# Optimization experiments

Hardware: AMD Instinct MI355X
Metric: run time of the kernel (lower is better)

## Reference

```python
import jax, jax.numpy as jnp
import numpy as np

SEQ = 8192
IN_DIM = 1024
HIDDEN_DIM = 2048
N_EXPERTS = 8
TOPK = 2


def setup_inputs() -> dict:
    key = jax.random.key(0)
    ks = jax.random.split(key, 6)
    scale = 0.02
    inp = jax.random.normal(ks[0], (SEQ, IN_DIM), jnp.float32)
    weights = jax.random.uniform(ks[1], (SEQ, TOPK), jnp.float32)
    selections = jax.random.randint(ks[2], (SEQ, TOPK), 0, N_EXPERTS, jnp.int32)
    up_proj = jax.random.normal(ks[3], (HIDDEN_DIM * N_EXPERTS, IN_DIM), jnp.float32) * scale
    gate_proj = jax.random.normal(ks[4], (HIDDEN_DIM * N_EXPERTS, IN_DIM), jnp.float32) * scale
    down_proj = jax.random.normal(ks[5], (HIDDEN_DIM * N_EXPERTS, IN_DIM), jnp.float32) * scale
    return {"inp": inp, "weights": weights, "up_proj": up_proj,
            "gate_proj": gate_proj, "down_proj": down_proj, "selections": selections}


def reference(inp, weights, up_proj, gate_proj, down_proj, selections):
    seq, in_dim = inp.shape
    topk = selections.shape[-1]
    # dispatch: replicate each token topk times -> (seq*topk, in_dim)
    x = jnp.broadcast_to(inp[:, None, :], (seq, topk, in_dim)).reshape(-1, in_dim)
    e_ids = selections.reshape(-1)  # (seq*topk,) expert id per dispatched token
    W_up = up_proj.reshape(N_EXPERTS, HIDDEN_DIM, in_dim)
    W_gate = gate_proj.reshape(N_EXPERTS, HIDDEN_DIM, in_dim)
    W_down = down_proj.reshape(N_EXPERTS, HIDDEN_DIM, in_dim)
    out = jnp.zeros_like(x)
    # grouped (block-sparse) GEMM: loop over the small fixed expert set,
    # masking tokens not routed to this expert (gelu(0)*0 = 0, so math matches).
    for e in range(N_EXPERTS):
        mask = (e_ids == e)[:, None]
        xe = jnp.where(mask, x, 0.0)
        h = xe @ W_up[e].T        # (seq*topk, hidden)
        g = xe @ W_gate[e].T      # (seq*topk, hidden)
        out = out + jnp.where(mask, (jax.nn.gelu(g) * h) @ W_down[e], 0.0)
    # combine: weighted sum over topk expert outputs per token
    return (out.reshape(seq, topk, in_dim) * weights[:, :, None]).sum(axis=1)
```

## Files before the change

kernel.cpp:

```cpp
#include <hip/hip_runtime.h>


#define SEQ 8192
#define IN_DIM 1024
#define HID 2048
#define NEXP 8
#define TOPK 2
#define NSLOT (SEQ * TOPK)

#define BM 128
#define BK 64
#define BM1 256
#define MAX_T1 72

typedef unsigned short ushort_t;
typedef __bf16 bf16x8 __attribute__((ext_vector_type(8)));
typedef float f32x4 __attribute__((ext_vector_type(4)));

__device__ __forceinline__ ushort_t f2bf(float f) {
    union { float f; unsigned u; } v;
    v.f = f;
    unsigned r = v.u + 0x7FFFu + ((v.u >> 16) & 1u);
    return (ushort_t)(r >> 16);
}

__device__ __forceinline__ float gelu_tanh(float x) {
    float u = 0.7978845608028654f * x * (1.0f + 0.044715f * x * x);
    return x / (1.0f + __expf(-2.0f * u));
}

__device__ __forceinline__ void async16(const void* g, void* l) {
    __builtin_amdgcn_global_load_lds(
        (const __attribute__((address_space(1))) unsigned int*)g,
        (__attribute__((address_space(3))) unsigned int*)l, 16, 0, 0);
}

__global__ void cast_bf16_kernel(const float* __restrict__ in,
                                 ushort_t* __restrict__ out, int n) {
    int i = (blockIdx.x * blockDim.x + threadIdx.x) * 4;
    if (i >= n) return;
    float4 v = *(const float4*)(in + i);
    union { ushort_t u[4]; uint2 v; } o;
    o.u[0] = f2bf(v.x); o.u[1] = f2bf(v.y);
    o.u[2] = f2bf(v.z); o.u[3] = f2bf(v.w);
    *(uint2*)(out + i) = o.v;
}

__global__ void transpose_cast_kernel(const float* __restrict__ in,
                                      ushort_t* __restrict__ out) {
    __shared__ float tile[32][33];
    int e = blockIdx.z;
    int d0 = blockIdx.x * 32, h0 = blockIdx.y * 32;
    int tx = threadIdx.x & 31, ty = threadIdx.x >> 5;
    const float* src = in + (size_t)e * HID * IN_DIM;
    for (int j = 0; j < 32; j += 8)
        tile[ty + j][tx] = src[(size_t)(h0 + ty + j) * IN_DIM + d0 + tx];
    __syncthreads();
    ushort_t* dst = out + (size_t)e * IN_DIM * HID;
    for (int j = 0; j < 32; j += 8)
        dst[(size_t)(d0 + ty + j) * HID + h0 + tx] = f2bf(tile[tx][ty + j]);
}

__global__ void route_kernel(const int* __restrict__ sel,
                             const float* __restrict__ wts,
                             int* __restrict__ meta,
                             int* __restrict__ stok,
                             int* __restrict__ sinv) {
    __shared__ int lc[256][NEXP];
    __shared__ int tot[NEXP];
    __shared__ int s_off[NEXP + 1];
    int t = threadIdx.x;
    int cnt[NEXP];
#pragma unroll
    for (int e = 0; e < NEXP; e++) cnt[e] = 0;
    int base = t * (NSLOT / 256);
    for (int i = 0; i < NSLOT / 256; i++) cnt[sel[base + i]]++;
#pragma unroll
    for (int e = 0; e < NEXP; e++) lc[t][e] = cnt[e];
    __syncthreads();
    if (t < NEXP) {
        int run = 0;
        for (int i = 0; i < 256; i++) { int v = lc[i][t]; lc[i][t] = run; run += v; }
        tot[t] = run;
    }
    __syncthreads();
    if (t == 0) {
        int o = 0;
        for (int e = 0; e < NEXP; e++) { s_off[e] = o; o += tot[e]; }
        s_off[NEXP] = o;
        for (int e = 0; e <= NEXP; e++) meta[e] = s_off[e];
        int nt = 0;
        for (int e = 0; e < NEXP; e++) {
            int c = s_off[e + 1] - s_off[e];
            int m = (c + BM - 1) / BM;
            for (int i = 0; i < m; i++) { meta[32 + 2 * nt] = e; meta[33 + 2 * nt] = i; nt++; }
        }
        meta[16] = nt;
    }
    __syncthreads();
    int cur[NEXP];
#pragma unroll
    for (int e = 0; e < NEXP; e++) cur[e] = s_off[e] + lc[t][e];
    for (int i = 0; i < NSLOT / 256; i++) {
        int slot = base + i;
        int e = sel[slot];
        int pos = cur[e]++;
        stok[pos] = slot >> 1;
        sinv[slot] = pos;
    }
}

#define ST_A(b, h, koff) {                                                 \
        async16(pA[h][0] + (koff), &AT[b][h][(w * 16) * BK]);              \
        async16(pA[h][1] + (koff), &AT[b][h][(w * 16 + 8) * BK]); }
#define ST_U(b, koff) {                                                    \
        async16(pU[0] + (koff), &UT[b][(w * 16) * BK]);                    \
        async16(pU[1] + (koff), &UT[b][(w * 16 + 8) * BK]); }
#define ST_G(b, koff) {                                                    \
        async16(pG[0] + (koff), &GT[b][(w * 16) * BK]);                    \
        async16(pG[1] + (koff), &GT[b][(w * 16 + 8) * BK]); }

#define RD_A(b, mb) {                                                      \
        _Pragma("unroll") for (int mi = 0; mi < 4; mi++)                   \
        _Pragma("unroll") for (int kh = 0; kh < 2; kh++)                   \
            a[mi][kh] = *(const bf16x8*)&AT[b][wm][                        \
                ((mb) + mi * 16 + r4) * BK + (((kh * 4 + q) ^ sw7) << 3)]; }
#define RD_U(b) {                                                          \
        _Pragma("unroll") for (int ni = 0; ni < 2; ni++)                   \
        _Pragma("unroll") for (int kh = 0; kh < 2; kh++)                   \
            bu[ni][kh] = *(const bf16x8*)&UT[b][                           \
                (wn * 32 + ni * 16 + r4) * BK + (((kh * 4 + q) ^ sw7) << 3)]; }
#define RD_G(b) {                                                          \
        _Pragma("unroll") for (int ni = 0; ni < 2; ni++)                   \
        _Pragma("unroll") for (int kh = 0; kh < 2; kh++)                   \
            bg[ni][kh] = *(const bf16x8*)&GT[b][                           \
                (wn * 32 + ni * 16 + r4) * BK + (((kh * 4 + q) ^ sw7) << 3)]; }

#define MM(ACC, mb2, BB) {                                                 \
        _Pragma("unroll") for (int mi = 0; mi < 4; mi++)                   \
        _Pragma("unroll") for (int ni = 0; ni < 2; ni++)                   \
        _Pragma("unroll") for (int kh = 0; kh < 2; kh++)                   \
            ACC[(mb2) + mi][ni] = __builtin_amdgcn_mfma_f32_16x16x32_bf16( \
                a[mi][kh], BB[ni][kh], ACC[(mb2) + mi][ni], 0, 0, 0); }

#define BARRIER __builtin_amdgcn_s_barrier()
#define LGKM0 asm volatile("s_waitcnt lgkmcnt(0)" ::: "memory")
#define VMW2 asm volatile("s_waitcnt vmcnt(2)" ::: "memory")
#define VMW0 asm volatile("s_waitcnt vmcnt(0)" ::: "memory")
#define PRIO1 __builtin_amdgcn_s_setprio(1)
#define PRIO0 __builtin_amdgcn_s_setprio(0)

#define KPRO                                                               \
    ST_A(0, 0, 0); ST_A(0, 1, 0); ST_U(0, 0); ST_G(0, 0);                  \
    ST_A(1, 0, 64);                                                        \
    VMW2; BARRIER;

#define KBODY_FULL                                                         \
    RD_A(0, 0); RD_U(0); ST_A(1, 1, 64); BARRIER; LGKM0;                   \
    PRIO1; MM(accH, 0, bu); PRIO0; BARRIER;                                \
    RD_G(0); ST_U(1, 64); BARRIER; LGKM0;                                  \
    PRIO1; MM(accG, 0, bg); PRIO0; BARRIER;                                \
    RD_A(0, 64); ST_G(1, 64); BARRIER; LGKM0;                              \
    PRIO1; MM(accG, 4, bg); PRIO0; BARRIER;                                \
    ST_A(0, 0, 128); VMW2; BARRIER;                                        \
    PRIO1; MM(accH, 4, bu); PRIO0; BARRIER;                                \
    RD_A(1, 0); RD_U(1); ST_A(0, 1, 128); BARRIER; LGKM0;                  \
    PRIO1; MM(accH, 0, bu); PRIO0; BARRIER;                                \
    RD_G(1); ST_U(0, 128); BARRIER; LGKM0;                                 \
    PRIO1; MM(accG, 0, bg); PRIO0; BARRIER;                                \
    RD_A(1, 64); ST_G(0, 128); BARRIER; LGKM0;                             \
    PRIO1; MM(accG, 4, bg); PRIO0; BARRIER;                                \
    ST_A(1, 0, 192); VMW2; BARRIER;                                        \
    PRIO1; MM(accH, 4, bu); PRIO0; BARRIER;

#define KBODY_ADV {                                                        \
    pA[0][0] += 128; pA[0][1] += 128; pA[1][0] += 128; pA[1][1] += 128;    \
    pU[0] += 128; pU[1] += 128; pG[0] += 128; pG[1] += 128; }

#define KBODY_TAIL                                                         \
    RD_A(0, 0); RD_U(0); ST_A(1, 1, 64); BARRIER; LGKM0;                   \
    PRIO1; MM(accH, 0, bu); PRIO0; BARRIER;                                \
    RD_G(0); ST_U(1, 64); BARRIER; LGKM0;                                  \
    PRIO1; MM(accG, 0, bg); PRIO0; BARRIER;                                \
    RD_A(0, 64); ST_G(1, 64); BARRIER; LGKM0;                              \
    PRIO1; MM(accG, 4, bg); PRIO0; BARRIER;                                \
    VMW0; BARRIER;                                                         \
    PRIO1; MM(accH, 4, bu); PRIO0; BARRIER;                                \
    RD_A(1, 0); RD_U(1); BARRIER; LGKM0;                                   \
    PRIO1; MM(accH, 0, bu); PRIO0; BARRIER;                                \
    RD_G(1); BARRIER; LGKM0;                                               \
    PRIO1; MM(accG, 0, bg); PRIO0; BARRIER;                                \
    RD_A(1, 64); BARRIER; LGKM0;                                           \
    PRIO1; MM(accG, 4, bg); PRIO0; BARRIER;                                \
    PRIO1; MM(accH, 4, bu); PRIO0;

#define TILE_DERIVE(tile)                                                  \
    int e = -1, mt = 0, accT = 0;                                          \
    _Pragma("unroll")                                                      \
    for (int ee = 0; ee < NEXP; ee++) {                                    \
        int c = meta[ee + 1] - meta[ee];                                   \
        int m = (c + BM1 - 1) >> 8;                                        \
        if ((tile) >= accT && (tile) < accT + m) { e = ee; mt = (tile) - accT; } \
        accT += m;                                                         \
    }                                                                      \
    if (e < 0) return;                                                     \
    int off = meta[e];                                                     \
    int cnt = meta[e + 1] - off;                                           \
    int m0 = mt * BM1;

__global__ __launch_bounds__(512, 2) void gemm1_kernel(
    const ushort_t* __restrict__ X,
    const ushort_t* __restrict__ U,
    const ushort_t* __restrict__ G,
    const int* __restrict__ meta,
    const int* __restrict__ stok,
    ushort_t* __restrict__ act) {
    __shared__ __align__(16) ushort_t AT[2][2][128 * BK];
    __shared__ __align__(16) ushort_t UT[2][128 * BK];
    __shared__ __align__(16) ushort_t GT[2][128 * BK];
    __shared__ int s_tok[BM1];

    int id = blockIdx.x + MAX_T1 * blockIdx.y;
    int wi = (id & 7) * 144 + (id >> 3);
    int tile = wi % MAX_T1;
    int n0 = (wi / MAX_T1) * 128;

    TILE_DERIVE(tile);

    int tid = threadIdx.x;
    if (tid < BM1) {
        int r = m0 + tid;
        if (r >= cnt) r = cnt - 1;
        s_tok[tid] = stok[off + r];
    }
    __syncthreads();

    int lane = tid & 63;
    int w = tid >> 6;
    int wm = w >> 2;
    int wn = w & 3;
    int srow = lane >> 3;
    int schunk = lane & 7;
    int gchunk = schunk ^ srow;
    int r4 = lane & 15;
    int q = lane >> 4;
    int sw7 = r4 & 7;

    const ushort_t* pA[2][2];
#pragma unroll
    for (int h = 0; h < 2; h++)
#pragma unroll
        for (int j = 0; j < 2; j++) {
            int r = h * 128 + w * 16 + j * 8 + srow;
            pA[h][j] = X + (size_t)s_tok[r] * IN_DIM + gchunk * 8;
        }
    const ushort_t* Ue = U + ((size_t)e * HID + n0) * IN_DIM;
    const ushort_t* Ge = G + ((size_t)e * HID + n0) * IN_DIM;
    const ushort_t* pU[2];
    const ushort_t* pG[2];
#pragma unroll
    for (int j = 0; j < 2; j++) {
        int r = w * 16 + j * 8 + srow;
        pU[j] = Ue + (size_t)r * IN_DIM + gchunk * 8;
        pG[j] = Ge + (size_t)r * IN_DIM + gchunk * 8;
    }

    f32x4 accH[8][2], accG[8][2];
#pragma unroll
    for (int mi = 0; mi < 8; mi++)
#pragma unroll
        for (int ni = 0; ni < 2; ni++) {
            accH[mi][ni] = (f32x4){0.f, 0.f, 0.f, 0.f};
            accG[mi][ni] = (f32x4){0.f, 0.f, 0.f, 0.f};
        }

    bf16x8 a[4][2], bu[2][2], bg[2][2];

    KPRO;
#pragma unroll 1
    for (int i = 0; i < (IN_DIM / BK) / 2 - 1; ++i) {
        KBODY_FULL;
        KBODY_ADV;
    }
    KBODY_TAIL;

#pragma unroll
    for (int mf = 0; mf < 8; mf++) {
#pragma unroll
        for (int r = 0; r < 4; r++) {
            int row_local = wm * 128 + mf * 16 + q * 4 + r;
            int grow = m0 + row_local;
            if (grow >= cnt) continue;
            size_t orow = (size_t)(off + grow) * HID + n0 + wn * 32;
#pragma unroll
            for (int ni = 0; ni < 2; ni++) {
                float h = accH[mf][ni][r];
                float g = accG[mf][ni][r];
                act[orow + ni * 16 + r4] = f2bf(gelu_tanh(g) * h);
            }
        }
    }
}

__global__ __launch_bounds__(512, 2) void gemm2_kernel(
    const ushort_t* __restrict__ act,
    const ushort_t* __restrict__ DT,
    const int* __restrict__ meta,
    float* __restrict__ y) {
    __shared__ __align__(16) ushort_t AT[2][2][128 * BK];
    __shared__ __align__(16) ushort_t UT[2][128 * BK];
    __shared__ __align__(16) ushort_t GT[2][128 * BK];

    int id = blockIdx.x + MAX_T1 * blockIdx.y;
    int wi = (id & 7) * 36 + (id >> 3);
    int tile = wi % MAX_T1;
    int n0 = (wi / MAX_T1) * 256;

    TILE_DERIVE(tile);

    int tid = threadIdx.x;
    int lane = tid & 63;
    int w = tid >> 6;
    int wm = w >> 2;
    int wn = w & 3;
    int srow = lane >> 3;
    int schunk = lane & 7;
    int gchunk = schunk ^ srow;
    int r4 = lane & 15;
    int q = lane >> 4;
    int sw7 = r4 & 7;

    const ushort_t* Ae = act + (size_t)off * HID;
    const ushort_t* pA[2][2];
#pragma unroll
    for (int h = 0; h < 2; h++)
#pragma unroll
        for (int j = 0; j < 2; j++) {
            int ar = m0 + h * 128 + w * 16 + j * 8 + srow;
            if (ar >= cnt) ar = cnt - 1;
            pA[h][j] = Ae + (size_t)ar * HID + gchunk * 8;
        }
    const ushort_t* Be = DT + ((size_t)e * IN_DIM + n0) * HID;
    const ushort_t* pU[2];
    const ushort_t* pG[2];
#pragma unroll
    for (int j = 0; j < 2; j++) {
        int r = w * 16 + j * 8 + srow;
        pU[j] = Be + (size_t)r * HID + gchunk * 8;
        pG[j] = Be + (size_t)(128 + r) * HID + gchunk * 8;
    }

    f32x4 accH[8][2], accG[8][2];
#pragma unroll
    for (int mi = 0; mi < 8; mi++)
#pragma unroll
        for (int ni = 0; ni < 2; ni++) {
            accH[mi][ni] = (f32x4){0.f, 0.f, 0.f, 0.f};
            accG[mi][ni] = (f32x4){0.f, 0.f, 0.f, 0.f};
        }

    bf16x8 a[4][2], bu[2][2], bg[2][2];

    KPRO;
#pragma unroll 1
    for (int i = 0; i < (HID / BK) / 2 - 1; ++i) {
        KBODY_FULL;
        KBODY_ADV;
    }
    KBODY_TAIL;

#pragma unroll
    for (int mf = 0; mf < 8; mf++) {
#pragma unroll
        for (int r = 0; r < 4; r++) {
            int row_local = wm * 128 + mf * 16 + q * 4 + r;
            int grow = m0 + row_local;
            if (grow >= cnt) continue;
            float* orow = y + (size_t)(off + grow) * IN_DIM + n0 + wn * 32;
#pragma unroll
            for (int ni = 0; ni < 2; ni++) {
                orow[ni * 16 + r4] = accH[mf][ni][r];
                orow[128 + ni * 16 + r4] = accG[mf][ni][r];
            }
        }
    }
}

__global__ __launch_bounds__(256) void combine_kernel(
    const float* __restrict__ y,
    const float* __restrict__ wts,
    const int* __restrict__ sinv,
    float* __restrict__ out) {
    int tok = blockIdx.x;
    int c = threadIdx.x;
    int p0 = sinv[tok * 2], p1 = sinv[tok * 2 + 1];
    float w0 = wts[tok * 2], w1 = wts[tok * 2 + 1];
    float4 a = *(const float4*)(y + (size_t)p0 * IN_DIM + c * 4);
    float4 b = *(const float4*)(y + (size_t)p1 * IN_DIM + c * 4);
    float4 o;
    o.x = w0 * a.x + w1 * b.x;
    o.y = w0 * a.y + w1 * b.y;
    o.z = w0 * a.z + w1 * b.z;
    o.w = w0 * a.w + w1 * b.w;
    *(float4*)(out + (size_t)tok * IN_DIM + c * 4) = o;
}

extern "C" void kernel_launch(void* const* d_in, const int* in_sizes, int n_in,
                              void* d_out, int out_size, void* d_ws, size_t ws_size,
                              hipStream_t stream) {
    const float* inp  = (const float*)d_in[0];
    const float* wts  = (const float*)d_in[1];
    const float* up   = (const float*)d_in[2];
    const float* gate = (const float*)d_in[3];
    const float* down = (const float*)d_in[4];
    const int*   sel  = (const int*)d_in[5];
    float* out = (float*)d_out;

    char* ws = (char*)d_ws;
    ushort_t* inp_bf  = (ushort_t*)(ws);
    ushort_t* up_bf   = (ushort_t*)(ws + 16777216);
    ushort_t* gate_bf = (ushort_t*)(ws + 50331648);
    ushort_t* down_bf = (ushort_t*)(ws + 83886080);
    ushort_t* act     = (ushort_t*)(ws + 117440512);
    int*      stok    = (int*)(ws + 184549376);
    int*      sinv    = (int*)(ws + 184614912);
    int*      meta    = (int*)(ws + 184680448);
    float*    y       = (float*)(ws);

    cast_bf16_kernel<<<(SEQ * IN_DIM) / 1024, 256, 0, stream>>>(inp, inp_bf, SEQ * IN_DIM);
    cast_bf16_kernel<<<(NEXP * HID * IN_DIM) / 1024, 256, 0, stream>>>(up, up_bf, NEXP * HID * IN_DIM);
    cast_bf16_kernel<<<(NEXP * HID * IN_DIM) / 1024, 256, 0, stream>>>(gate, gate_bf, NEXP * HID * IN_DIM);
    transpose_cast_kernel<<<dim3(IN_DIM / 32, HID / 32, NEXP), 256, 0, stream>>>(down, down_bf);
    route_kernel<<<1, 256, 0, stream>>>(sel, wts, meta, stok, sinv);
    gemm1_kernel<<<dim3(MAX_T1, HID / 128), 512, 0, stream>>>(inp_bf, up_bf, gate_bf, meta, stok, act);
    gemm2_kernel<<<dim3(MAX_T1, IN_DIM / 256), 512, 0, stream>>>(act, down_bf, meta, y);
    combine_kernel<<<SEQ, 256, 0, stream>>>(y, wts, sinv, out);
}
```

Baseline: 567.1 us.

## Fuse cast kernels, issue whole-tile prefetches, and remap blocks to XCDs

Merges the three fp32-to-bf16 cast launches into one kernel, which removes two kernel launches. Both GEMM loops now issue the full next-tile global-to-LDS prefetch in one batch and wait with vmcnt(8), instead of spreading the loads between MFMA phases. The block-to-tile mapping in gemm1 and gemm2 is changed so that blocks sharing a token tile or an expert's weights land on the same XCD, aiming for better L2 reuse. Issuing loads in a batch may cost some overlap of memory traffic with compute.

Result: slower. 605.8 us (+6.8%).

```diff
diff --git a/kernel.cpp b/kernel.cpp
--- a/kernel.cpp
+++ b/kernel.cpp
@@ -35,15 +35,25 @@
         (__attribute__((address_space(3))) unsigned int*)l, 16, 0, 0);
 }
 
-__global__ void cast_bf16_kernel(const float* __restrict__ in,
-                                 ushort_t* __restrict__ out, int n) {
-    int i = (blockIdx.x * blockDim.x + threadIdx.x) * 4;
-    if (i >= n) return;
-    float4 v = *(const float4*)(in + i);
+__global__ void cast3_kernel(const float* __restrict__ inp,
+                             const float* __restrict__ up,
+                             const float* __restrict__ gate,
+                             ushort_t* __restrict__ o_inp,
+                             ushort_t* __restrict__ o_up,
+                             ushort_t* __restrict__ o_gate) {
+    const int N1 = SEQ * IN_DIM;
+    const int N2 = NEXP * HID * IN_DIM;
+    long i = (long)(blockIdx.x * blockDim.x + threadIdx.x) * 4;
+    const float* src;
+    ushort_t* dst;
+    if (i < N1)            { src = inp  + i;            dst = o_inp  + i; }
+    else if (i < N1 + N2)  { src = up   + (i - N1);     dst = o_up   + (i - N1); }
+    else                   { src = gate + (i - N1 - N2); dst = o_gate + (i - N1 - N2); }
+    float4 v = *(const float4*)src;
     union { ushort_t u[4]; uint2 v; } o;
     o.u[0] = f2bf(v.x); o.u[1] = f2bf(v.y);
     o.u[2] = f2bf(v.z); o.u[3] = f2bf(v.w);
-    *(uint2*)(out + i) = o.v;
+    *(uint2*)dst = o.v;
 }
 
 __global__ void transpose_cast_kernel(const float* __restrict__ in,
@@ -119,6 +129,8 @@
 #define ST_G(b, koff) {                                                    \
         async16(pG[0] + (koff), &GT[b][(w * 16) * BK]);                    \
         async16(pG[1] + (koff), &GT[b][(w * 16 + 8) * BK]); }
+#define ST_TILE(b, koff) { ST_A(b, 0, koff); ST_A(b, 1, koff);             \
+                           ST_U(b, koff);    ST_G(b, koff); }
 
 #define RD_A(b, mb) {                                                      \
         _Pragma("unroll") for (int mi = 0; mi < 4; mi++)                   \
@@ -145,32 +157,31 @@
 
 #define BARRIER __builtin_amdgcn_s_barrier()
 #define LGKM0 asm volatile("s_waitcnt lgkmcnt(0)" ::: "memory")
-#define VMW2 asm volatile("s_waitcnt vmcnt(2)" ::: "memory")
+#define VMW8 asm volatile("s_waitcnt vmcnt(8)" ::: "memory")
 #define VMW0 asm volatile("s_waitcnt vmcnt(0)" ::: "memory")
 #define PRIO1 __builtin_amdgcn_s_setprio(1)
 #define PRIO0 __builtin_amdgcn_s_setprio(0)
 
 #define KPRO                                                               \
-    ST_A(0, 0, 0); ST_A(0, 1, 0); ST_U(0, 0); ST_G(0, 0);                  \
-    ST_A(1, 0, 64);                                                        \
-    VMW2; BARRIER;
+    ST_TILE(0, 0); ST_TILE(1, 64);                                         \
+    VMW8; BARRIER;
 
 #define KBODY_FULL                                                         \
-    RD_A(0, 0); RD_U(0); ST_A(1, 1, 64); BARRIER; LGKM0;                   \
+    RD_A(0, 0); RD_U(0); BARRIER; LGKM0;                                   \
     PRIO1; MM(accH, 0, bu); PRIO0; BARRIER;                                \
-    RD_G(0); ST_U(1, 64); BARRIER; LGKM0;                                  \
+    RD_G(0); BARRIER; LGKM0;                                               \
     PRIO1; MM(accG, 0, bg); PRIO0; BARRIER;                                \
-    RD_A(0, 64); ST_G(1, 64); BARRIER; LGKM0;                              \
+    RD_A(0, 64); BARRIER; LGKM0;                                           \
     PRIO1; MM(accG, 4, bg); PRIO0; BARRIER;                                \
-    ST_A(0, 0, 128); VMW2; BARRIER;                                        \
+    ST_TILE(0, 128); VMW8; BARRIER;                                        \
     PRIO1; MM(accH, 4, bu); PRIO0; BARRIER;                                \
-    RD_A(1, 0); RD_U(1); ST_A(0, 1, 128); BARRIER; LGKM0;                  \
+    RD_A(1, 0); RD_U(1); BARRIER; LGKM0;                                   \
     PRIO1; MM(accH, 0, bu); PRIO0; BARRIER;                                \
-    RD_G(1); ST_U(0, 128); BARRIER; LGKM0;                                 \
+    RD_G(1); BARRIER; LGKM0;                                               \
     PRIO1; MM(accG, 0, bg); PRIO0; BARRIER;                                \
-    RD_A(1, 64); ST_G(0, 128); BARRIER; LGKM0;                             \
+    RD_A(1, 64); BARRIER; LGKM0;                                           \
     PRIO1; MM(accG, 4, bg); PRIO0; BARRIER;                                \
-    ST_A(1, 0, 192); VMW2; BARRIER;                                        \
+    ST_TILE(1, 192); VMW8; BARRIER;                                        \
     PRIO1; MM(accH, 4, bu); PRIO0; BARRIER;
 
 #define KBODY_ADV {                                                        \
@@ -178,11 +189,11 @@
     pU[0] += 128; pU[1] += 128; pG[0] += 128; pG[1] += 128; }
 
 #define KBODY_TAIL                                                         \
-    RD_A(0, 0); RD_U(0); ST_A(1, 1, 64); BARRIER; LGKM0;                   \
+    RD_A(0, 0); RD_U(0); BARRIER; LGKM0;                                   \
     PRIO1; MM(accH, 0, bu); PRIO0; BARRIER;                                \
-    RD_G(0); ST_U(1, 64); BARRIER; LGKM0;                                  \
+    RD_G(0); BARRIER; LGKM0;                                               \
     PRIO1; MM(accG, 0, bg); PRIO0; BARRIER;                                \
-    RD_A(0, 64); ST_G(1, 64); BARRIER; LGKM0;                              \
+    RD_A(0, 64); BARRIER; LGKM0;                                           \
     PRIO1; MM(accG, 4, bg); PRIO0; BARRIER;                                \
     VMW0; BARRIER;                                                         \
     PRIO1; MM(accH, 4, bu); PRIO0; BARRIER;                                \
@@ -221,9 +232,10 @@
     __shared__ int s_tok[BM1];
 
     int id = blockIdx.x + MAX_T1 * blockIdx.y;
-    int wi = (id & 7) * 144 + (id >> 3);
-    int tile = wi % MAX_T1;
-    int n0 = (wi / MAX_T1) * 128;
+    int xcd = id & 7;
+    int j = id >> 3;
+    int tile = j >> 1;
+    int n0 = ((xcd << 1) | (j & 1)) * 128;
 
     TILE_DERIVE(tile);
 
@@ -250,19 +262,19 @@
 #pragma unroll
     for (int h = 0; h < 2; h++)
 #pragma unroll
-        for (int j = 0; j < 2; j++) {
-            int r = h * 128 + w * 16 + j * 8 + srow;
-            pA[h][j] = X + (size_t)s_tok[r] * IN_DIM + gchunk * 8;
+        for (int jj = 0; jj < 2; jj++) {
+            int r = h * 128 + w * 16 + jj * 8 + srow;
+            pA[h][jj] = X + (size_t)s_tok[r] * IN_DIM + gchunk * 8;
         }
     const ushort_t* Ue = U + ((size_t)e * HID + n0) * IN_DIM;
     const ushort_t* Ge = G + ((size_t)e * HID + n0) * IN_DIM;
     const ushort_t* pU[2];
     const ushort_t* pG[2];
 #pragma unroll
-    for (int j = 0; j < 2; j++) {
-        int r = w * 16 + j * 8 + srow;
-        pU[j] = Ue + (size_t)r * IN_DIM + gchunk * 8;
-        pG[j] = Ge + (size_t)r * IN_DIM + gchunk * 8;
+    for (int jj = 0; jj < 2; jj++) {
+        int r = w * 16 + jj * 8 + srow;
+        pU[jj] = Ue + (size_t)r * IN_DIM + gchunk * 8;
+        pG[jj] = Ge + (size_t)r * IN_DIM + gchunk * 8;
     }
 
     f32x4 accH[8][2], accG[8][2];
@@ -312,9 +324,10 @@
     __shared__ __align__(16) ushort_t GT[2][128 * BK];
 
     int id = blockIdx.x + MAX_T1 * blockIdx.y;
-    int wi = (id & 7) * 36 + (id >> 3);
-    int tile = wi % MAX_T1;
-    int n0 = (wi / MAX_T1) * 256;
+    int xcd = id & 7;
+    int j = id >> 3;
+    int tile = xcd * 9 + (j >> 2);
+    int n0 = (j & 3) * 256;
 
     TILE_DERIVE(tile);
 
@@ -335,19 +348,19 @@
 #pragma unroll
     for (int h = 0; h < 2; h++)
 #pragma unroll
-        for (int j = 0; j < 2; j++) {
-            int ar = m0 + h * 128 + w * 16 + j * 8 + srow;
+        for (int jj = 0; jj < 2; jj++) {
+            int ar = m0 + h * 128 + w * 16 + jj * 8 + srow;
             if (ar >= cnt) ar = cnt - 1;
-            pA[h][j] = Ae + (size_t)ar * HID + gchunk * 8;
+            pA[h][jj] = Ae + (size_t)ar * HID + gchunk * 8;
         }
     const ushort_t* Be = DT + ((size_t)e * IN_DIM + n0) * HID;
     const ushort_t* pU[2];
     const ushort_t* pG[2];
 #pragma unroll
-    for (int j = 0; j < 2; j++) {
-        int r = w * 16 + j * 8 + srow;
-        pU[j] = Be + (size_t)r * HID + gchunk * 8;
-        pG[j] = Be + (size_t)(128 + r) * HID + gchunk * 8;
+    for (int jj = 0; jj < 2; jj++) {
+        int r = w * 16 + jj * 8 + srow;
+        pU[jj] = Be + (size_t)r * HID + gchunk * 8;
+        pG[jj] = Be + (size_t)(128 + r) * HID + gchunk * 8;
     }
 
     f32x4 accH[8][2], accG[8][2];
@@ -427,9 +440,9 @@
     int*      meta    = (int*)(ws + 184680448);
     float*    y       = (float*)(ws);
 
-    cast_bf16_kernel<<<(SEQ * IN_DIM) / 1024, 256, 0, stream>>>(inp, inp_bf, SEQ * IN_DIM);
-    cast_bf16_kernel<<<(NEXP * HID * IN_DIM) / 1024, 256, 0, stream>>>(up, up_bf, NEXP * HID * IN_DIM);
-    cast_bf16_kernel<<<(NEXP * HID * IN_DIM) / 1024, 256, 0, stream>>>(gate, gate_bf, NEXP * HID * IN_DIM);
+    const int CAST_N = SEQ * IN_DIM + 2 * NEXP * HID * IN_DIM;
+    cast3_kernel<<<CAST_N / 1024, 256, 0, stream>>>(inp, up, gate,
+                                                    inp_bf, up_bf, gate_bf);
     transpose_cast_kernel<<<dim3(IN_DIM / 32, HID / 32, NEXP), 256, 0, stream>>>(down, down_bf);
     route_kernel<<<1, 256, 0, stream>>>(sel, wts, meta, stok, sinv);
     gemm1_kernel<<<dim3(MAX_T1, HID / 128), 512, 0, stream>>>(inp_bf, up_bf, gate_bf, meta, stok, act);
```
